# Performance work log

Hardware: AMD Instinct MI355X
Metric: run time of the kernel (lower is better)

## Reference

```python
import jax, jax.numpy as jnp
import numpy as np

N_NODES = 50000
N_EDGES = 1600000
NUM_FEATURES = 128
HIDDEN = 32
HEADS = 4
NUM_CLASSES = 32
NEG_SLOPE = 0.2


def setup_inputs() -> dict:
    key = jax.random.key(0)
    ks = jax.random.split(key, 10)
    glorot = lambda k, shp: jax.random.normal(k, shp, jnp.float32) * jnp.sqrt(2.0 / (shp[0] + shp[-1]))
    return {
        "x": jax.random.normal(ks[0], (N_NODES, NUM_FEATURES), jnp.float32),
        "edge_index": jax.random.randint(ks[1], (2, N_EDGES), 0, N_NODES, jnp.int32),
        "W1": glorot(ks[2], (NUM_FEATURES, HEADS * HIDDEN)),
        "att_src1": glorot(ks[3], (HEADS, HIDDEN)),
        "att_dst1": glorot(ks[4], (HEADS, HIDDEN)),
        "b1": jnp.zeros((HEADS * HIDDEN,), jnp.float32),
        "W2": glorot(ks[5], (HEADS * HIDDEN, NUM_CLASSES)),
        "att_src2": glorot(ks[6], (1, NUM_CLASSES)),
        "att_dst2": glorot(ks[7], (1, NUM_CLASSES)),
        "b2": jnp.zeros((NUM_CLASSES,), jnp.float32),
    }


def _leaky_relu(v):
    return jnp.where(v >= 0, v, NEG_SLOPE * v)


def _gat_conv(x, src, dst, W, att_src, att_dst, bias, heads, ch, concat):
    # x: [N, F_in]; src/dst: [E] (self-loops already included)
    n = x.shape[0]
    h = (x @ W).reshape(n, heads, ch)                    # [N, H, C]
    a_src = jnp.sum(h * att_src[None], axis=-1)          # [N, H]
    a_dst = jnp.sum(h * att_dst[None], axis=-1)          # [N, H]
    e = _leaky_relu(a_src[src] + a_dst[dst])             # [E, H]
    # segment softmax over incoming edges of each dst node
    mx = jax.ops.segment_max(e, dst, num_segments=n)     # [N, H]
    mx = jnp.where(jnp.isfinite(mx), mx, 0.0)
    mx = jax.lax.stop_gradient(mx)
    ex = jnp.exp(e - mx[dst])                            # [E, H]
    den = jax.ops.segment_sum(ex, dst, num_segments=n)   # [N, H]
    alpha = ex / (den[dst] + 1e-16)                      # [E, H]
    out = jax.ops.segment_sum(h[src] * alpha[:, :, None], dst, num_segments=n)  # [N, H, C]
    if concat:
        out = out.reshape(n, heads * ch)
    else:
        out = out.mean(axis=1)
    return out + bias


def _add_self_loops(edge_index, n):
    loops = jnp.arange(n, dtype=edge_index.dtype)
    src = jnp.concatenate([edge_index[0], loops])
    dst = jnp.concatenate([edge_index[1], loops])
    return src, dst


def reference(x, edge_index, W1, att_src1, att_dst1, b1, W2, att_src2, att_dst2, b2):
    src, dst = _add_self_loops(edge_index, x.shape[0])
    h = _gat_conv(x, src, dst, W1, att_src1, att_dst1, b1, HEADS, HIDDEN, True)
    h = jax.nn.relu(h)
    out = _gat_conv(h, src, dst, W2, att_src2, att_dst2, b2, 1, NUM_CLASSES, False)
    return jax.nn.softmax(out, axis=1)
```

## Files before the change

### kernel.cpp

```cpp
#include <hip/hip_runtime.h>
#include <math.h>

#define HEADS 4
#define HID 32
#define FEAT 128
#define NCLS 32
#define NS 0.2f
#define CHUNK 4096
#define BSTRIDE 12288

__device__ __forceinline__ unsigned short f2bf(float x) {
    unsigned u = __float_as_uint(x);
    unsigned r = (u + 0x7FFFu + ((u >> 16) & 1u)) >> 16;
    return (unsigned short)r;
}
__device__ __forceinline__ float2 bf2x2(unsigned u) {
    float2 r;
    r.x = __uint_as_float(u << 16);
    r.y = __uint_as_float(u & 0xFFFF0000u);
    return r;
}

__device__ __forceinline__ void scan256(int* arr, int tid, int* wsum) {
    int v = arr[tid];
    int incl = v;
    #pragma unroll
    for (int off = 1; off < 64; off <<= 1) {
        int t = __shfl_up(incl, off, 64);
        if ((tid & 63) >= off) incl += t;
    }
    int wid = tid >> 6;
    if ((tid & 63) == 63) wsum[wid] = incl;
    __syncthreads();
    int wpre = 0;
    #pragma unroll
    for (int w = 0; w < 3; ++w) if (w < wid) wpre += wsum[w];
    arr[tid] = wpre + incl - v;
    __syncthreads();
}


__global__ __launch_bounds__(256) void cursor_init_kernel(int* __restrict__ gcursor) {
    gcursor[threadIdx.x] = threadIdx.x * BSTRIDE;
}

__global__ __launch_bounds__(256) void bin_kernel(
    const int* __restrict__ ei, int E, int ET,
    int* __restrict__ gcursor, unsigned int* __restrict__ binned) {
    __shared__ int hist[256];
    __shared__ int lcur[256];
    __shared__ int rbase[256];
    __shared__ int wsum[4];
    __shared__ unsigned int stage[CHUNK];
    __shared__ unsigned short sbkt[CHUNK];
    int tid = threadIdx.x;
    int cb = blockIdx.x * CHUNK;
    int sv[16], dv[16];
    hist[tid] = 0;
    __syncthreads();
    #pragma unroll
    for (int r = 0; r < 16; ++r) {
        int i = cb + r * 256 + tid;
        int s = 0, d = -1;
        if (i < ET) {
            if (i < E) { s = ei[i]; d = ei[E + i]; }
            else { s = d = i - E; }
            atomicAdd(&hist[d >> 8], 1);
        }
        sv[r] = s; dv[r] = d;
    }
    __syncthreads();
    int c = hist[tid];
    rbase[tid] = c ? atomicAdd(&gcursor[tid], c) : 0;
    scan256(hist, tid, wsum);
    lcur[tid] = hist[tid];
    __syncthreads();
    #pragma unroll
    for (int r = 0; r < 16; ++r) {
        if (dv[r] >= 0) {
            int b = dv[r] >> 8;
            int slot = atomicAdd(&lcur[b], 1);
            stage[slot] = (unsigned int)sv[r] | ((unsigned int)(dv[r] & 255) << 16);
            sbkt[slot] = (unsigned short)b;
        }
    }
    __syncthreads();
    int nval = ET - cb; if (nval > CHUNK) nval = CHUNK;
    for (int j = tid; j < nval; j += 256) {
        int b = sbkt[j];
        binned[rbase[b] + (j - hist[b])] = stage[j];
    }
}

__global__ __launch_bounds__(256) void csr_kernel(
    unsigned int* __restrict__ binned, const int* __restrict__ gcursor,
    int* __restrict__ offs, int* __restrict__ oend, int N) {
    __shared__ int ncnt[256];
    __shared__ int ncur[256];
    __shared__ int wsum[4];
    __shared__ unsigned short lcsr[BSTRIDE];
    int b = blockIdx.x, tid = threadIdx.x;
    int base = b * BSTRIDE;
    int cnt = gcursor[b] - base;
    if (cnt > BSTRIDE) cnt = BSTRIDE;
    ncnt[tid] = 0;
    __syncthreads();
    for (int j = tid; j < cnt; j += 256)
        atomicAdd(&ncnt[(binned[base + j] >> 16) & 255], 1);
    __syncthreads();
    int c = ncnt[tid];
    __syncthreads();
    scan256(ncnt, tid, wsum);
    int pre = ncnt[tid];
    int g = (b << 8) + tid;
    if (g < N) { offs[g] = base + pre; oend[g] = base + pre + c; }
    ncur[tid] = pre;
    __syncthreads();
    for (int j = tid; j < cnt; j += 256) {
        unsigned int u = binned[base + j];
        int p = atomicAdd(&ncur[(u >> 16) & 255], 1);
        lcsr[p] = (unsigned short)(u & 0xFFFFu);
    }
    __syncthreads();
    for (int j = tid; j < cnt; j += 256)
        binned[base + j] = (unsigned int)lcsr[j];
}

__global__ __launch_bounds__(256) void gemm1_kernel(
    const float* __restrict__ x, const float* __restrict__ W1,
    const float* __restrict__ as1, const float* __restrict__ ad1,
    unsigned short* __restrict__ h1b, float* __restrict__ a1s,
    float* __restrict__ a1d, int N) {
    __shared__ float xs[64][32];
    __shared__ float ws[32][128];
    int tid = threadIdx.x;
    int tx = tid & 31;
    int ty = tid >> 5;
    int row0 = blockIdx.x * 64;
    float4 acc[8];
    #pragma unroll
    for (int r = 0; r < 8; ++r) acc[r] = make_float4(0.f, 0.f, 0.f, 0.f);

    for (int k0 = 0; k0 < FEAT; k0 += 32) {
        __syncthreads();
        #pragma unroll
        for (int i = tid; i < 512; i += 256) {
            int r = i >> 3, c4 = i & 7;
            int n = row0 + r;
            float4 v = (n < N) ? *(const float4*)(x + (size_t)n * FEAT + k0 + c4 * 4)
                               : make_float4(0.f, 0.f, 0.f, 0.f);
            *(float4*)&xs[r][c4 * 4] = v;
        }
        #pragma unroll
        for (int i = tid; i < 1024; i += 256) {
            int k = i >> 5, c4 = i & 31;
            *(float4*)&ws[k][c4 * 4] =
                *(const float4*)(W1 + (size_t)(k0 + k) * FEAT + c4 * 4);
        }
        __syncthreads();

        for (int k = 0; k < 32; k += 4) {
            float4 xv[8];
            #pragma unroll
            for (int r = 0; r < 8; ++r) xv[r] = *(float4*)&xs[ty * 8 + r][k];
            #pragma unroll
            for (int kk = 0; kk < 4; ++kk) {
                float4 wv = *(float4*)&ws[k + kk][tx * 4];
                #pragma unroll
                for (int r = 0; r < 8; ++r) {
                    float xr = (kk == 0) ? xv[r].x : (kk == 1) ? xv[r].y
                             : (kk == 2) ? xv[r].z : xv[r].w;
                    acc[r].x += xr * wv.x;
                    acc[r].y += xr * wv.y;
                    acc[r].z += xr * wv.z;
                    acc[r].w += xr * wv.w;
                }
            }
        }
    }
    int hd = tx >> 3;
    float4 av = *(const float4*)(as1 + tx * 4);
    float4 dv = *(const float4*)(ad1 + tx * 4);
    #pragma unroll
    for (int r = 0; r < 8; ++r) {
        int n = row0 + ty * 8 + r;
        if (n >= N) break;
        unsigned int lo = (unsigned)f2bf(acc[r].x) | ((unsigned)f2bf(acc[r].y) << 16);
        unsigned int hi = (unsigned)f2bf(acc[r].z) | ((unsigned)f2bf(acc[r].w) << 16);
        uint2 pk; pk.x = lo; pk.y = hi;
        *(uint2*)(h1b + (size_t)n * FEAT + tx * 4) = pk;
        float vs = acc[r].x * av.x + acc[r].y * av.y + acc[r].z * av.z + acc[r].w * av.w;
        float vd = acc[r].x * dv.x + acc[r].y * dv.y + acc[r].z * dv.z + acc[r].w * dv.w;
        #pragma unroll
        for (int off = 4; off; off >>= 1) {
            vs += __shfl_down(vs, off);
            vd += __shfl_down(vd, off);
        }
        if ((tx & 7) == 0) {
            a1s[n * HEADS + hd] = vs;
            a1d[n * HEADS + hd] = vd;
        }
    }
}

__global__ __launch_bounds__(256) void agg1_kernel(
    const unsigned short* __restrict__ h1b, const float* __restrict__ a1s,
    const float* __restrict__ a1d, const int* __restrict__ offs,
    const int* __restrict__ oend, const int* __restrict__ csr,
    const float* __restrict__ b1, float* __restrict__ hout, int N) {
    int d = blockIdx.x * 4 + (threadIdx.x >> 6);
    if (d >= N) return;
    int lane = threadIdx.x & 63;
    int beg = offs[d], end = oend[d];
    int q = lane >> 4, sub = lane & 15;
    int cl = sub * 8;
    int h3 = sub >> 2;
    float adh = a1d[d * 4 + h3];
    float dn = 0.f;
    float2 c0 = {0.f, 0.f}, c1 = {0.f, 0.f}, c2 = {0.f, 0.f}, c3 = {0.f, 0.f};
    for (int i = beg; i < end; i += 16) {
        int i0 = i + q, i1 = i + 4 + q, i2 = i + 8 + q, i3 = i + 12 + q;
        bool v0 = i0 < end, v1 = i1 < end, v2 = i2 < end, v3 = i3 < end;
        int s0 = csr[v0 ? i0 : beg];
        int s1 = csr[v1 ? i1 : beg];
        int s2 = csr[v2 ? i2 : beg];
        int s3 = csr[v3 ? i3 : beg];
        float e0 = a1s[s0 * 4 + h3] + adh; e0 = e0 >= 0.f ? e0 : NS * e0;
        float e1 = a1s[s1 * 4 + h3] + adh; e1 = e1 >= 0.f ? e1 : NS * e1;
        float e2 = a1s[s2 * 4 + h3] + adh; e2 = e2 >= 0.f ? e2 : NS * e2;
        float e3 = a1s[s3 * 4 + h3] + adh; e3 = e3 >= 0.f ? e3 : NS * e3;
        float al0 = v0 ? __expf(e0) : 0.f;
        float al1 = v1 ? __expf(e1) : 0.f;
        float al2 = v2 ? __expf(e2) : 0.f;
        float al3 = v3 ? __expf(e3) : 0.f;
        dn += (al0 + al1) + (al2 + al3);
        uint4 A = *(const uint4*)(h1b + (size_t)s0 * FEAT + cl);
        uint4 B = *(const uint4*)(h1b + (size_t)s1 * FEAT + cl);
        uint4 C = *(const uint4*)(h1b + (size_t)s2 * FEAT + cl);
        uint4 D = *(const uint4*)(h1b + (size_t)s3 * FEAT + cl);
        float2 t;
        t = bf2x2(A.x); c0.x += t.x * al0; c0.y += t.y * al0;
        t = bf2x2(A.y); c1.x += t.x * al0; c1.y += t.y * al0;
        t = bf2x2(A.z); c2.x += t.x * al0; c2.y += t.y * al0;
        t = bf2x2(A.w); c3.x += t.x * al0; c3.y += t.y * al0;
        t = bf2x2(B.x); c0.x += t.x * al1; c0.y += t.y * al1;
        t = bf2x2(B.y); c1.x += t.x * al1; c1.y += t.y * al1;
        t = bf2x2(B.z); c2.x += t.x * al1; c2.y += t.y * al1;
        t = bf2x2(B.w); c3.x += t.x * al1; c3.y += t.y * al1;
        t = bf2x2(C.x); c0.x += t.x * al2; c0.y += t.y * al2;
        t = bf2x2(C.y); c1.x += t.x * al2; c1.y += t.y * al2;
        t = bf2x2(C.z); c2.x += t.x * al2; c2.y += t.y * al2;
        t = bf2x2(C.w); c3.x += t.x * al2; c3.y += t.y * al2;
        t = bf2x2(D.x); c0.x += t.x * al3; c0.y += t.y * al3;
        t = bf2x2(D.y); c1.x += t.x * al3; c1.y += t.y * al3;
        t = bf2x2(D.z); c2.x += t.x * al3; c2.y += t.y * al3;
        t = bf2x2(D.w); c3.x += t.x * al3; c3.y += t.y * al3;
    }
    dn += __shfl_xor(dn, 16);
    dn += __shfl_xor(dn, 32);
    #pragma unroll
    for (int off = 32; off >= 16; off >>= 1) {
        c0.x += __shfl_xor(c0.x, off); c0.y += __shfl_xor(c0.y, off);
        c1.x += __shfl_xor(c1.x, off); c1.y += __shfl_xor(c1.y, off);
        c2.x += __shfl_xor(c2.x, off); c2.y += __shfl_xor(c2.y, off);
        c3.x += __shfl_xor(c3.x, off); c3.y += __shfl_xor(c3.y, off);
    }
    if (q == 0) {
        float inv = 1.0f / (dn + 1e-16f);
        float4 b0 = *(const float4*)(b1 + cl);
        float4 b4 = *(const float4*)(b1 + cl + 4);
        float4 o0, o1;
        o0.x = c0.x * inv + b0.x; o0.x = o0.x > 0.f ? o0.x : 0.f;
        o0.y = c0.y * inv + b0.y; o0.y = o0.y > 0.f ? o0.y : 0.f;
        o0.z = c1.x * inv + b0.z; o0.z = o0.z > 0.f ? o0.z : 0.f;
        o0.w = c1.y * inv + b0.w; o0.w = o0.w > 0.f ? o0.w : 0.f;
        o1.x = c2.x * inv + b4.x; o1.x = o1.x > 0.f ? o1.x : 0.f;
        o1.y = c2.y * inv + b4.y; o1.y = o1.y > 0.f ? o1.y : 0.f;
        o1.z = c3.x * inv + b4.z; o1.z = o1.z > 0.f ? o1.z : 0.f;
        o1.w = c3.y * inv + b4.w; o1.w = o1.w > 0.f ? o1.w : 0.f;
        *(float4*)(hout + (size_t)d * FEAT + cl) = o0;
        *(float4*)(hout + (size_t)d * FEAT + cl + 4) = o1;
    }
}

__global__ __launch_bounds__(256) void gemm2_kernel(
    const float* __restrict__ h, const float* __restrict__ W2,
    const float* __restrict__ as2, const float* __restrict__ ad2,
    unsigned short* __restrict__ g2b, float* __restrict__ a2s,
    float* __restrict__ a2d, int N) {
    __shared__ float xs[128][33];
    __shared__ float ws[FEAT][NCLS];
    int tid = threadIdx.x;
    int tx = tid & 7;
    int ty = tid >> 3;
    int row0 = blockIdx.x * 128;

    #pragma unroll
    for (int i = tid; i < FEAT * NCLS / 4; i += 256) {
        int k = i >> 3, c4 = i & 7;
        *(float4*)&ws[k][c4 * 4] = *(const float4*)(W2 + (size_t)k * NCLS + c4 * 4);
    }

    float4 acc[4];
    #pragma unroll
    for (int r = 0; r < 4; ++r) acc[r] = make_float4(0.f, 0.f, 0.f, 0.f);

    for (int k0 = 0; k0 < FEAT; k0 += 32) {
        __syncthreads();
        #pragma unroll
        for (int i = tid; i < 1024; i += 256) {
            int r = i >> 3, c4 = i & 7;
            int n = row0 + r;
            float4 v = (n < N) ? *(const float4*)(h + (size_t)n * FEAT + k0 + c4 * 4)
                               : make_float4(0.f, 0.f, 0.f, 0.f);
            xs[r][c4 * 4 + 0] = v.x;
            xs[r][c4 * 4 + 1] = v.y;
            xs[r][c4 * 4 + 2] = v.z;
            xs[r][c4 * 4 + 3] = v.w;
        }
        __syncthreads();

        for (int k = 0; k < 32; k += 4) {
            #pragma unroll
            for (int kk = 0; kk < 4; ++kk) {
                float4 wv = *(float4*)&ws[k0 + k + kk][tx * 4];
                #pragma unroll
                for (int r = 0; r < 4; ++r) {
                    float xr = xs[ty * 4 + r][k + kk];
                    acc[r].x += xr * wv.x;
                    acc[r].y += xr * wv.y;
                    acc[r].z += xr * wv.z;
                    acc[r].w += xr * wv.w;
                }
            }
        }
    }
    float4 av = *(const float4*)(as2 + tx * 4);
    float4 dv = *(const float4*)(ad2 + tx * 4);
    #pragma unroll
    for (int r = 0; r < 4; ++r) {
        int n = row0 + ty * 4 + r;
        if (n >= N) break;
        unsigned int lo = (unsigned)f2bf(acc[r].x) | ((unsigned)f2bf(acc[r].y) << 16);
        unsigned int hi = (unsigned)f2bf(acc[r].z) | ((unsigned)f2bf(acc[r].w) << 16);
        uint2 pk; pk.x = lo; pk.y = hi;
        *(uint2*)(g2b + (size_t)n * NCLS + tx * 4) = pk;
        float vs = acc[r].x * av.x + acc[r].y * av.y + acc[r].z * av.z + acc[r].w * av.w;
        float vd = acc[r].x * dv.x + acc[r].y * dv.y + acc[r].z * dv.z + acc[r].w * dv.w;
        #pragma unroll
        for (int off = 4; off; off >>= 1) {
            vs += __shfl_down(vs, off);
            vd += __shfl_down(vd, off);
        }
        if (tx == 0) { a2s[n] = vs; a2d[n] = vd; }
    }
}

__global__ __launch_bounds__(256) void agg2_kernel(
    const unsigned short* __restrict__ g2b, const float* __restrict__ a2s,
    const float* __restrict__ a2d, const int* __restrict__ offs,
    const int* __restrict__ oend, const int* __restrict__ csr,
    const float* __restrict__ b2, float* __restrict__ out, int N) {
    int d = blockIdx.x * 4 + (threadIdx.x >> 6);
    if (d >= N) return;
    int lane = threadIdx.x & 63;
    int beg = offs[d], end = oend[d];
    float ad = a2d[d];

    int q = lane >> 4, sub = lane & 15;
    int ch2 = sub * 2;
    float dn = 0.f;
    float2 ac = {0.f, 0.f};
    for (int i = beg; i < end; i += 16) {
        int i0 = i + q, i1 = i + 4 + q, i2 = i + 8 + q, i3 = i + 12 + q;
        bool v0 = i0 < end, v1 = i1 < end, v2 = i2 < end, v3 = i3 < end;
        int s0 = csr[v0 ? i0 : beg];
        int s1 = csr[v1 ? i1 : beg];
        int s2 = csr[v2 ? i2 : beg];
        int s3 = csr[v3 ? i3 : beg];
        float e0 = a2s[s0] + ad; e0 = e0 >= 0.f ? e0 : NS * e0;
        float e1 = a2s[s1] + ad; e1 = e1 >= 0.f ? e1 : NS * e1;
        float e2 = a2s[s2] + ad; e2 = e2 >= 0.f ? e2 : NS * e2;
        float e3 = a2s[s3] + ad; e3 = e3 >= 0.f ? e3 : NS * e3;
        float al0 = v0 ? __expf(e0) : 0.f;
        float al1 = v1 ? __expf(e1) : 0.f;
        float al2 = v2 ? __expf(e2) : 0.f;
        float al3 = v3 ? __expf(e3) : 0.f;
        dn += (al0 + al1) + (al2 + al3);
        unsigned int A = *(const unsigned int*)(g2b + (size_t)s0 * NCLS + ch2);
        unsigned int B = *(const unsigned int*)(g2b + (size_t)s1 * NCLS + ch2);
        unsigned int C = *(const unsigned int*)(g2b + (size_t)s2 * NCLS + ch2);
        unsigned int D = *(const unsigned int*)(g2b + (size_t)s3 * NCLS + ch2);
        float2 t;
        t = bf2x2(A); ac.x += t.x * al0; ac.y += t.y * al0;
        t = bf2x2(B); ac.x += t.x * al1; ac.y += t.y * al1;
        t = bf2x2(C); ac.x += t.x * al2; ac.y += t.y * al2;
        t = bf2x2(D); ac.x += t.x * al3; ac.y += t.y * al3;
    }
    dn += __shfl_xor(dn, 16);
    dn += __shfl_xor(dn, 32);
    #pragma unroll
    for (int off = 32; off >= 16; off >>= 1) {
        ac.x += __shfl_xor(ac.x, off);
        ac.y += __shfl_xor(ac.y, off);
    }
    float inv = 1.0f / (dn + 1e-16f);
    float2 bb = *(const float2*)(b2 + ch2);
    float v0 = ac.x * inv + bb.x;
    float v1 = ac.y * inv + bb.y;
    float m = fmaxf(v0, v1);
    #pragma unroll
    for (int off = 8; off; off >>= 1) m = fmaxf(m, __shfl_xor(m, off, 16));
    float e0 = __expf(v0 - m), e1 = __expf(v1 - m);
    float sm = e0 + e1;
    #pragma unroll
    for (int off = 8; off; off >>= 1) sm += __shfl_xor(sm, off, 16);
    if (q == 0) {
        float2 o; o.x = e0 / sm; o.y = e1 / sm;
        *(float2*)(out + (size_t)d * NCLS + ch2) = o;
    }
}

extern "C" void kernel_launch(void* const* d_in, const int* in_sizes, int n_in,
                              void* d_out, int out_size, void* d_ws, size_t ws_size,
                              hipStream_t stream) {
    const float* x   = (const float*)d_in[0];
    const int*   ei  = (const int*)d_in[1];
    const float* W1  = (const float*)d_in[2];
    const float* as1 = (const float*)d_in[3];
    const float* ad1 = (const float*)d_in[4];
    const float* b1  = (const float*)d_in[5];
    const float* W2  = (const float*)d_in[6];
    const float* as2 = (const float*)d_in[7];
    const float* ad2 = (const float*)d_in[8];
    const float* b2  = (const float*)d_in[9];
    float* out = (float*)d_out;

    int N = in_sizes[0] / FEAT;
    int E = in_sizes[1] / 2;
    int ET = E + N;
    int NB = (N + 255) >> 8;

    float* ws   = (float*)d_ws;
    unsigned short* h1b = (unsigned short*)ws;
    float* hout = (float*)(h1b + (size_t)N * FEAT);
    unsigned short* g2b = (unsigned short*)(hout + (size_t)N * FEAT);
    float* a1s  = (float*)(g2b + (size_t)N * NCLS);
    float* a1d  = a1s + (size_t)N * HEADS;
    float* a2s  = a1d + (size_t)N * HEADS;
    float* a2d  = a2s + N;
    int* offs   = (int*)(a2d + N);
    int* oend   = offs + N;
    unsigned int* binned = (unsigned int*)(oend + N);
    int* gcursor = (int*)(binned + (size_t)256 * BSTRIDE);

    int nchunks = (ET + CHUNK - 1) / CHUNK;

    cursor_init_kernel<<<1, 256, 0, stream>>>(gcursor);
    bin_kernel<<<nchunks, 256, 0, stream>>>(ei, E, ET, gcursor, binned);
    csr_kernel<<<NB, 256, 0, stream>>>(binned, gcursor, offs, oend, N);

    const int* csr = (const int*)binned;
    gemm1_kernel<<<(N + 63) / 64, 256, 0, stream>>>(x, W1, as1, ad1, h1b, a1s, a1d, N);
    agg1_kernel<<<(N + 3) / 4, 256, 0, stream>>>(h1b, a1s, a1d, offs, oend, csr, b1, hout, N);
    gemm2_kernel<<<(N + 127) / 128, 256, 0, stream>>>(hout, W2, as2, ad2, g2b, a2s, a2d, N);
    agg2_kernel<<<(N + 3) / 4, 256, 0, stream>>>(g2b, a2s, a2d, offs, oend, csr, b2, out, N);
}
```

Baseline: 261.8 us.

## Fuse gemm1 with edge binning and precompute per-edge attention weights in agg1

Merges the first GEMM and the edge-binning pass into one launch, with blocks split by index and shared memory overlaid through a union, so the two independent stages run concurrently and one launch is dropped. In agg1, nodes with degree up to 64 now compute all four head exponentials once per edge per lane, stage them and the source indices in shared memory, and reduce the softmax denominator with shuffles. This replaces the old scheme where each lane recomputed the exponential for its own head from global memory. Higher-degree nodes keep the old loop. The costs are a block barrier in agg1 and more shared memory, which may lower occupancy.

```diff
diff --git a/kernel.cpp b/kernel.cpp
--- a/kernel.cpp
+++ b/kernel.cpp
@@ -39,104 +39,25 @@
     __syncthreads();
 }
 
-
 __global__ __launch_bounds__(256) void cursor_init_kernel(int* __restrict__ gcursor) {
     gcursor[threadIdx.x] = threadIdx.x * BSTRIDE;
 }
 
-__global__ __launch_bounds__(256) void bin_kernel(
-    const int* __restrict__ ei, int E, int ET,
-    int* __restrict__ gcursor, unsigned int* __restrict__ binned) {
-    __shared__ int hist[256];
-    __shared__ int lcur[256];
-    __shared__ int rbase[256];
-    __shared__ int wsum[4];
-    __shared__ unsigned int stage[CHUNK];
-    __shared__ unsigned short sbkt[CHUNK];
-    int tid = threadIdx.x;
-    int cb = blockIdx.x * CHUNK;
-    int sv[16], dv[16];
-    hist[tid] = 0;
-    __syncthreads();
-    #pragma unroll
-    for (int r = 0; r < 16; ++r) {
-        int i = cb + r * 256 + tid;
-        int s = 0, d = -1;
-        if (i < ET) {
-            if (i < E) { s = ei[i]; d = ei[E + i]; }
-            else { s = d = i - E; }
-            atomicAdd(&hist[d >> 8], 1);
-        }
-        sv[r] = s; dv[r] = d;
-    }
-    __syncthreads();
-    int c = hist[tid];
-    rbase[tid] = c ? atomicAdd(&gcursor[tid], c) : 0;
-    scan256(hist, tid, wsum);
-    lcur[tid] = hist[tid];
-    __syncthreads();
-    #pragma unroll
-    for (int r = 0; r < 16; ++r) {
-        if (dv[r] >= 0) {
-            int b = dv[r] >> 8;
-            int slot = atomicAdd(&lcur[b], 1);
-            stage[slot] = (unsigned int)sv[r] | ((unsigned int)(dv[r] & 255) << 16);
-            sbkt[slot] = (unsigned short)b;
-        }
-    }
-    __syncthreads();
-    int nval = ET - cb; if (nval > CHUNK) nval = CHUNK;
-    for (int j = tid; j < nval; j += 256) {
-        int b = sbkt[j];
-        binned[rbase[b] + (j - hist[b])] = stage[j];
-    }
-}
-
-__global__ __launch_bounds__(256) void csr_kernel(
-    unsigned int* __restrict__ binned, const int* __restrict__ gcursor,
-    int* __restrict__ offs, int* __restrict__ oend, int N) {
-    __shared__ int ncnt[256];
-    __shared__ int ncur[256];
-    __shared__ int wsum[4];
-    __shared__ unsigned short lcsr[BSTRIDE];
-    int b = blockIdx.x, tid = threadIdx.x;
-    int base = b * BSTRIDE;
-    int cnt = gcursor[b] - base;
-    if (cnt > BSTRIDE) cnt = BSTRIDE;
-    ncnt[tid] = 0;
-    __syncthreads();
-    for (int j = tid; j < cnt; j += 256)
-        atomicAdd(&ncnt[(binned[base + j] >> 16) & 255], 1);
-    __syncthreads();
-    int c = ncnt[tid];
-    __syncthreads();
-    scan256(ncnt, tid, wsum);
-    int pre = ncnt[tid];
-    int g = (b << 8) + tid;
-    if (g < N) { offs[g] = base + pre; oend[g] = base + pre + c; }
-    ncur[tid] = pre;
-    __syncthreads();
-    for (int j = tid; j < cnt; j += 256) {
-        unsigned int u = binned[base + j];
-        int p = atomicAdd(&ncur[(u >> 16) & 255], 1);
-        lcsr[p] = (unsigned short)(u & 0xFFFFu);
-    }
-    __syncthreads();
-    for (int j = tid; j < cnt; j += 256)
-        binned[base + j] = (unsigned int)lcsr[j];
-}
-
-__global__ __launch_bounds__(256) void gemm1_kernel(
+union SMem {
+    struct { float xs[64][32]; float ws[32][128]; } g;
+    struct { int hist[256]; int lcur[256]; int rbase[256]; int wsum[4];
+             unsigned int stage[CHUNK]; unsigned short sbkt[CHUNK]; } b;
+};
+
+__device__ void gemm1_body(SMem& sm, int bid,
     const float* __restrict__ x, const float* __restrict__ W1,
     const float* __restrict__ as1, const float* __restrict__ ad1,
     unsigned short* __restrict__ h1b, float* __restrict__ a1s,
     float* __restrict__ a1d, int N) {
-    __shared__ float xs[64][32];
-    __shared__ float ws[32][128];
     int tid = threadIdx.x;
     int tx = tid & 31;
     int ty = tid >> 5;
-    int row0 = blockIdx.x * 64;
+    int row0 = bid * 64;
     float4 acc[8];
     #pragma unroll
     for (int r = 0; r < 8; ++r) acc[r] = make_float4(0.f, 0.f, 0.f, 0.f);
@@ -149,12 +70,12 @@
             int n = row0 + r;
             float4 v = (n < N) ? *(const float4*)(x + (size_t)n * FEAT + k0 + c4 * 4)
                                : make_float4(0.f, 0.f, 0.f, 0.f);
-            *(float4*)&xs[r][c4 * 4] = v;
+            *(float4*)&sm.g.xs[r][c4 * 4] = v;
         }
         #pragma unroll
         for (int i = tid; i < 1024; i += 256) {
             int k = i >> 5, c4 = i & 31;
-            *(float4*)&ws[k][c4 * 4] =
+            *(float4*)&sm.g.ws[k][c4 * 4] =
                 *(const float4*)(W1 + (size_t)(k0 + k) * FEAT + c4 * 4);
         }
         __syncthreads();
@@ -162,10 +83,10 @@
         for (int k = 0; k < 32; k += 4) {
             float4 xv[8];
             #pragma unroll
-            for (int r = 0; r < 8; ++r) xv[r] = *(float4*)&xs[ty * 8 + r][k];
+            for (int r = 0; r < 8; ++r) xv[r] = *(float4*)&sm.g.xs[ty * 8 + r][k];
             #pragma unroll
             for (int kk = 0; kk < 4; ++kk) {
-                float4 wv = *(float4*)&ws[k + kk][tx * 4];
+                float4 wv = *(float4*)&sm.g.ws[k + kk][tx * 4];
                 #pragma unroll
                 for (int r = 0; r < 8; ++r) {
                     float xr = (kk == 0) ? xv[r].x : (kk == 1) ? xv[r].y
@@ -203,61 +124,220 @@
     }
 }
 
+__device__ void bin_body(SMem& sm, int bid,
+    const int* __restrict__ ei, int E, int ET,
+    int* __restrict__ gcursor, unsigned int* __restrict__ binned) {
+    int tid = threadIdx.x;
+    int cb = bid * CHUNK;
+    int sv[16], dv[16];
+    sm.b.hist[tid] = 0;
+    __syncthreads();
+    #pragma unroll
+    for (int r = 0; r < 16; ++r) {
+        int i = cb + r * 256 + tid;
+        int s = 0, d = -1;
+        if (i < ET) {
+            if (i < E) { s = ei[i]; d = ei[E + i]; }
+            else { s = d = i - E; }
+            atomicAdd(&sm.b.hist[d >> 8], 1);
+        }
+        sv[r] = s; dv[r] = d;
+    }
+    __syncthreads();
+    int c = sm.b.hist[tid];
+    sm.b.rbase[tid] = c ? atomicAdd(&gcursor[tid], c) : 0;
+    scan256(sm.b.hist, tid, sm.b.wsum);
+    sm.b.lcur[tid] = sm.b.hist[tid];
+    __syncthreads();
+    #pragma unroll
+    for (int r = 0; r < 16; ++r) {
+        if (dv[r] >= 0) {
+            int b = dv[r] >> 8;
+            int slot = atomicAdd(&sm.b.lcur[b], 1);
+            sm.b.stage[slot] = (unsigned int)sv[r] | ((unsigned int)(dv[r] & 255) << 16);
+            sm.b.sbkt[slot] = (unsigned short)b;
+        }
+    }
+    __syncthreads();
+    int nval = ET - cb; if (nval > CHUNK) nval = CHUNK;
+    for (int j = tid; j < nval; j += 256) {
+        int b = sm.b.sbkt[j];
+        binned[sm.b.rbase[b] + (j - sm.b.hist[b])] = sm.b.stage[j];
+    }
+}
+
+__global__ __launch_bounds__(256) void fat1_kernel(
+    int g1blocks,
+    const float* __restrict__ x, const float* __restrict__ W1,
+    const float* __restrict__ as1, const float* __restrict__ ad1,
+    unsigned short* __restrict__ h1b, float* __restrict__ a1s,
+    float* __restrict__ a1d, int N,
+    const int* __restrict__ ei, int E, int ET,
+    int* __restrict__ gcursor, unsigned int* __restrict__ binned) {
+    __shared__ SMem sm;
+    if ((int)blockIdx.x < g1blocks)
+        gemm1_body(sm, blockIdx.x, x, W1, as1, ad1, h1b, a1s, a1d, N);
+    else
+        bin_body(sm, blockIdx.x - g1blocks, ei, E, ET, gcursor, binned);
+}
+
+__global__ __launch_bounds__(256) void csr_kernel(
+    unsigned int* __restrict__ binned, const int* __restrict__ gcursor,
+    int* __restrict__ offs, int* __restrict__ oend, int N) {
+    __shared__ int ncnt[256];
+    __shared__ int ncur[256];
+    __shared__ int wsum[4];
+    __shared__ unsigned short lcsr[BSTRIDE];
+    int b = blockIdx.x, tid = threadIdx.x;
+    int base = b * BSTRIDE;
+    int cnt = gcursor[b] - base;
+    if (cnt > BSTRIDE) cnt = BSTRIDE;
+    ncnt[tid] = 0;
+    __syncthreads();
+    for (int j = tid; j < cnt; j += 256)
+        atomicAdd(&ncnt[(binned[base + j] >> 16) & 255], 1);
+    __syncthreads();
+    int c = ncnt[tid];
+    __syncthreads();
+    scan256(ncnt, tid, wsum);
+    int pre = ncnt[tid];
+    int g = (b << 8) + tid;
+    if (g < N) { offs[g] = base + pre; oend[g] = base + pre + c; }
+    ncur[tid] = pre;
+    __syncthreads();
+    for (int j = tid; j < cnt; j += 256) {
+        unsigned int u = binned[base + j];
+        int p = atomicAdd(&ncur[(u >> 16) & 255], 1);
+        lcsr[p] = (unsigned short)(u & 0xFFFFu);
+    }
+    __syncthreads();
+    for (int j = tid; j < cnt; j += 256)
+        binned[base + j] = (unsigned int)lcsr[j];
+}
+
 __global__ __launch_bounds__(256) void agg1_kernel(
     const unsigned short* __restrict__ h1b, const float* __restrict__ a1s,
     const float* __restrict__ a1d, const int* __restrict__ offs,
     const int* __restrict__ oend, const int* __restrict__ csr,
     const float* __restrict__ b1, float* __restrict__ hout, int N) {
-    int d = blockIdx.x * 4 + (threadIdx.x >> 6);
-    if (d >= N) return;
+    __shared__ float exs[4][64][4];
+    __shared__ int   sN[4][64];
+    int wv = threadIdx.x >> 6;
+    int d = blockIdx.x * 4 + wv;
+    bool active = (d < N);
     int lane = threadIdx.x & 63;
-    int beg = offs[d], end = oend[d];
+    int beg = 0, end = 0, deg = 0;
+    float4 adv = make_float4(0.f, 0.f, 0.f, 0.f);
+    if (active) {
+        beg = offs[d]; end = oend[d]; deg = end - beg;
+        adv = *(const float4*)(a1d + d * 4);
+    }
+
+    float al0 = 0.f, al1 = 0.f, al2 = 0.f, al3 = 0.f;
+    int s_e = 0;
+    if (active && lane < deg && deg <= 64) {
+        s_e = csr[beg + lane];
+        float4 as = *(const float4*)(a1s + s_e * 4);
+        float e0 = as.x + adv.x; e0 = e0 >= 0.f ? e0 : NS * e0; al0 = __expf(e0);
+        float e1 = as.y + adv.y; e1 = e1 >= 0.f ? e1 : NS * e1; al1 = __expf(e1);
+        float e2 = as.z + adv.z; e2 = e2 >= 0.f ? e2 : NS * e2; al2 = __expf(e2);
+        float e3 = as.w + adv.w; e3 = e3 >= 0.f ? e3 : NS * e3; al3 = __expf(e3);
+    }
+    sN[wv][lane] = s_e;
+    *(float4*)&exs[wv][lane][0] = make_float4(al0, al1, al2, al3);
+    __syncthreads();
+    if (!active) return;
+
     int q = lane >> 4, sub = lane & 15;
     int cl = sub * 8;
     int h3 = sub >> 2;
-    float adh = a1d[d * 4 + h3];
-    float dn = 0.f;
     float2 c0 = {0.f, 0.f}, c1 = {0.f, 0.f}, c2 = {0.f, 0.f}, c3 = {0.f, 0.f};
-    for (int i = beg; i < end; i += 16) {
-        int i0 = i + q, i1 = i + 4 + q, i2 = i + 8 + q, i3 = i + 12 + q;
-        bool v0 = i0 < end, v1 = i1 < end, v2 = i2 < end, v3 = i3 < end;
-        int s0 = csr[v0 ? i0 : beg];
-        int s1 = csr[v1 ? i1 : beg];
-        int s2 = csr[v2 ? i2 : beg];
-        int s3 = csr[v3 ? i3 : beg];
-        float e0 = a1s[s0 * 4 + h3] + adh; e0 = e0 >= 0.f ? e0 : NS * e0;
-        float e1 = a1s[s1 * 4 + h3] + adh; e1 = e1 >= 0.f ? e1 : NS * e1;
-        float e2 = a1s[s2 * 4 + h3] + adh; e2 = e2 >= 0.f ? e2 : NS * e2;
-        float e3 = a1s[s3 * 4 + h3] + adh; e3 = e3 >= 0.f ? e3 : NS * e3;
-        float al0 = v0 ? __expf(e0) : 0.f;
-        float al1 = v1 ? __expf(e1) : 0.f;
-        float al2 = v2 ? __expf(e2) : 0.f;
-        float al3 = v3 ? __expf(e3) : 0.f;
-        dn += (al0 + al1) + (al2 + al3);
-        uint4 A = *(const uint4*)(h1b + (size_t)s0 * FEAT + cl);
-        uint4 B = *(const uint4*)(h1b + (size_t)s1 * FEAT + cl);
-        uint4 C = *(const uint4*)(h1b + (size_t)s2 * FEAT + cl);
-        uint4 D = *(const uint4*)(h1b + (size_t)s3 * FEAT + cl);
-        float2 t;
-        t = bf2x2(A.x); c0.x += t.x * al0; c0.y += t.y * al0;
-        t = bf2x2(A.y); c1.x += t.x * al0; c1.y += t.y * al0;
-        t = bf2x2(A.z); c2.x += t.x * al0; c2.y += t.y * al0;
-        t = bf2x2(A.w); c3.x += t.x * al0; c3.y += t.y * al0;
-        t = bf2x2(B.x); c0.x += t.x * al1; c0.y += t.y * al1;
-        t = bf2x2(B.y); c1.x += t.x * al1; c1.y += t.y * al1;
-        t = bf2x2(B.z); c2.x += t.x * al1; c2.y += t.y * al1;
-        t = bf2x2(B.w); c3.x += t.x * al1; c3.y += t.y * al1;
-        t = bf2x2(C.x); c0.x += t.x * al2; c0.y += t.y * al2;
-        t = bf2x2(C.y); c1.x += t.x * al2; c1.y += t.y * al2;
-        t = bf2x2(C.z); c2.x += t.x * al2; c2.y += t.y * al2;
-        t = bf2x2(C.w); c3.x += t.x * al2; c3.y += t.y * al2;
-        t = bf2x2(D.x); c0.x += t.x * al3; c0.y += t.y * al3;
-        t = bf2x2(D.y); c1.x += t.x * al3; c1.y += t.y * al3;
-        t = bf2x2(D.z); c2.x += t.x * al3; c2.y += t.y * al3;
-        t = bf2x2(D.w); c3.x += t.x * al3; c3.y += t.y * al3;
-    }
-    dn += __shfl_xor(dn, 16);
-    dn += __shfl_xor(dn, 32);
+    float inv;
+
+    if (deg <= 64) {
+        float dn0 = al0, dn1 = al1, dn2 = al2, dn3 = al3;
+        #pragma unroll
+        for (int off = 32; off; off >>= 1) {
+            dn0 += __shfl_xor(dn0, off);
+            dn1 += __shfl_xor(dn1, off);
+            dn2 += __shfl_xor(dn2, off);
+            dn3 += __shfl_xor(dn3, off);
+        }
+        float dnh = (h3 == 0) ? dn0 : (h3 == 1) ? dn1 : (h3 == 2) ? dn2 : dn3;
+        inv = 1.0f / (dnh + 1e-16f);
+        for (int e = q; e < deg; e += 16) {
+            int e1i = e + 4, e2i = e + 8, e3i = e + 12;
+            int s0 = sN[wv][e],   s1 = sN[wv][e1i];
+            int s2 = sN[wv][e2i], s3 = sN[wv][e3i];
+            float a0 = exs[wv][e][h3],   a1 = exs[wv][e1i][h3];
+            float a2 = exs[wv][e2i][h3], a3 = exs[wv][e3i][h3];
+            uint4 A = *(const uint4*)(h1b + (size_t)s0 * FEAT + cl);
+            uint4 B = *(const uint4*)(h1b + (size_t)s1 * FEAT + cl);
+            uint4 C = *(const uint4*)(h1b + (size_t)s2 * FEAT + cl);
+            uint4 D = *(const uint4*)(h1b + (size_t)s3 * FEAT + cl);
+            float2 t;
+            t = bf2x2(A.x); c0.x += t.x * a0; c0.y += t.y * a0;
+            t = bf2x2(A.y); c1.x += t.x * a0; c1.y += t.y * a0;
+            t = bf2x2(A.z); c2.x += t.x * a0; c2.y += t.y * a0;
+            t = bf2x2(A.w); c3.x += t.x * a0; c3.y += t.y * a0;
+            t = bf2x2(B.x); c0.x += t.x * a1; c0.y += t.y * a1;
+            t = bf2x2(B.y); c1.x += t.x * a1; c1.y += t.y * a1;
+            t = bf2x2(B.z); c2.x += t.x * a1; c2.y += t.y * a1;
+            t = bf2x2(B.w); c3.x += t.x * a1; c3.y += t.y * a1;
+            t = bf2x2(C.x); c0.x += t.x * a2; c0.y += t.y * a2;
+            t = bf2x2(C.y); c1.x += t.x * a2; c1.y += t.y * a2;
+            t = bf2x2(C.z); c2.x += t.x * a2; c2.y += t.y * a2;
+            t = bf2x2(C.w); c3.x += t.x * a2; c3.y += t.y * a2;
+            t = bf2x2(D.x); c0.x += t.x * a3; c0.y += t.y * a3;
+            t = bf2x2(D.y); c1.x += t.x * a3; c1.y += t.y * a3;
+            t = bf2x2(D.z); c2.x += t.x * a3; c2.y += t.y * a3;
+            t = bf2x2(D.w); c3.x += t.x * a3; c3.y += t.y * a3;
+        }
+    } else {
+        float adh = (h3 == 0) ? adv.x : (h3 == 1) ? adv.y : (h3 == 2) ? adv.z : adv.w;
+        float dn = 0.f;
+        for (int i = beg; i < end; i += 16) {
+            int i0 = i + q, i1 = i + 4 + q, i2 = i + 8 + q, i3 = i + 12 + q;
+            bool v0 = i0 < end, v1 = i1 < end, v2 = i2 < end, v3 = i3 < end;
+            int s0 = csr[v0 ? i0 : beg];
+            int s1 = csr[v1 ? i1 : beg];
+            int s2 = csr[v2 ? i2 : beg];
+            int s3 = csr[v3 ? i3 : beg];
+            float e0 = a1s[s0 * 4 + h3] + adh; e0 = e0 >= 0.f ? e0 : NS * e0;
+            float e1 = a1s[s1 * 4 + h3] + adh; e1 = e1 >= 0.f ? e1 : NS * e1;
+            float e2 = a1s[s2 * 4 + h3] + adh; e2 = e2 >= 0.f ? e2 : NS * e2;
+            float e3 = a1s[s3 * 4 + h3] + adh; e3 = e3 >= 0.f ? e3 : NS * e3;
+            float al0f = v0 ? __expf(e0) : 0.f;
+            float al1f = v1 ? __expf(e1) : 0.f;
+            float al2f = v2 ? __expf(e2) : 0.f;
+            float al3f = v3 ? __expf(e3) : 0.f;
+            dn += (al0f + al1f) + (al2f + al3f);
+            uint4 A = *(const uint4*)(h1b + (size_t)s0 * FEAT + cl);
+            uint4 B = *(const uint4*)(h1b + (size_t)s1 * FEAT + cl);
+            uint4 C = *(const uint4*)(h1b + (size_t)s2 * FEAT + cl);
+            uint4 D = *(const uint4*)(h1b + (size_t)s3 * FEAT + cl);
+            float2 t;
+            t = bf2x2(A.x); c0.x += t.x * al0f; c0.y += t.y * al0f;
+            t = bf2x2(A.y); c1.x += t.x * al0f; c1.y += t.y * al0f;
+            t = bf2x2(A.z); c2.x += t.x * al0f; c2.y += t.y * al0f;
+            t = bf2x2(A.w); c3.x += t.x * al0f; c3.y += t.y * al0f;
+            t = bf2x2(B.x); c0.x += t.x * al1f; c0.y += t.y * al1f;
+            t = bf2x2(B.y); c1.x += t.x * al1f; c1.y += t.y * al1f;
+            t = bf2x2(B.z); c2.x += t.x * al1f; c2.y += t.y * al1f;
+            t = bf2x2(B.w); c3.x += t.x * al1f; c3.y += t.y * al1f;
+            t = bf2x2(C.x); c0.x += t.x * al2f; c0.y += t.y * al2f;
+            t = bf2x2(C.y); c1.x += t.x * al2f; c1.y += t.y * al2f;
+            t = bf2x2(C.z); c2.x += t.x * al2f; c2.y += t.y * al2f;
+            t = bf2x2(C.w); c3.x += t.x * al2f; c3.y += t.y * al2f;
+            t = bf2x2(D.x); c0.x += t.x * al3f; c0.y += t.y * al3f;
+            t = bf2x2(D.y); c1.x += t.x * al3f; c1.y += t.y * al3f;
+            t = bf2x2(D.z); c2.x += t.x * al3f; c2.y += t.y * al3f;
+            t = bf2x2(D.w); c3.x += t.x * al3f; c3.y += t.y * al3f;
+        }
+        dn += __shfl_xor(dn, 16);
+        dn += __shfl_xor(dn, 32);
+        inv = 1.0f / (dn + 1e-16f);
+    }
     #pragma unroll
     for (int off = 32; off >= 16; off >>= 1) {
         c0.x += __shfl_xor(c0.x, off); c0.y += __shfl_xor(c0.y, off);
@@ -266,7 +346,6 @@
         c3.x += __shfl_xor(c3.x, off); c3.y += __shfl_xor(c3.y, off);
     }
     if (q == 0) {
-        float inv = 1.0f / (dn + 1e-16f);
         float4 b0 = *(const float4*)(b1 + cl);
         float4 b4 = *(const float4*)(b1 + cl + 4);
         float4 o0, o1;
@@ -455,13 +534,14 @@
     int* gcursor = (int*)(binned + (size_t)256 * BSTRIDE);
 
     int nchunks = (ET + CHUNK - 1) / CHUNK;
+    int g1blocks = (N + 63) / 64;
 
     cursor_init_kernel<<<1, 256, 0, stream>>>(gcursor);
-    bin_kernel<<<nchunks, 256, 0, stream>>>(ei, E, ET, gcursor, binned);
+    fat1_kernel<<<g1blocks + nchunks, 256, 0, stream>>>(
+        g1blocks, x, W1, as1, ad1, h1b, a1s, a1d, N, ei, E, ET, gcursor, binned);
     csr_kernel<<<NB, 256, 0, stream>>>(binned, gcursor, offs, oend, N);
 
     const int* csr = (const int*)binned;
-    gemm1_kernel<<<(N + 63) / 64, 256, 0, stream>>>(x, W1, as1, ad1, h1b, a1s, a1d, N);
     agg1_kernel<<<(N + 3) / 4, 256, 0, stream>>>(h1b, a1s, a1d, offs, oend, csr, b1, hout, N);
     gemm2_kernel<<<(N + 127) / 128, 256, 0, stream>>>(hout, W2, as2, ad2, g2b, a2s, a2d, N);
     agg2_kernel<<<(N + 3) / 4, 256, 0, stream>>>(g2b, a2s, a2d, offs, oend, csr, b2, out, N);
```

Result: no change. 266.2 us (+1.7%).
